# Optimization experiments

Measured on AMD Instinct MI355X. Metric: run time of the kernel, lower is better.

Reference implementation:

```python
import jax, jax.numpy as jnp
import numpy as np

B, F, N, D = 4, 5, 2048, 256


def setup_inputs() -> dict:
    key = jax.random.key(0)
    k1, k2 = jax.random.split(key)
    x = jax.random.normal(k1, (B, F, N, D), dtype=jnp.float32)
    y = jax.random.normal(k2, (B, F, N, D), dtype=jnp.float32)
    return {"x": x, "y": y}


def _weight(a, b):
    # pairwise_distance with p=2 in the original is sum((a-b)**2)**(1/(2-1)),
    # i.e. SQUARED euclidean distance (no sqrt). Use gram expansion to avoid
    # materializing the [B,F,N,N,D] difference tensor.
    a2 = jnp.sum(a * a, axis=-1)                      # [B,F,N]
    b2 = jnp.sum(b * b, axis=-1)                      # [B,F,M]
    ab = jnp.einsum('bfnd,bfmd->bfnm', a, b)          # [B,F,N,M]
    d = a2[..., :, None] + b2[..., None, :] - 2.0 * ab  # squared dists
    # min over neighbors (dim=1 of the per-frame matrix), mean over query
    # nodes, then mean over frames -> one scalar per batch element.
    return jnp.mean(jnp.min(d, axis=-1), axis=(-1, -2))  # [B]


def _normalize(f):
    # min/max over the node dim (dim=2), per (batch, frame, feature)
    mn = jnp.min(f, axis=2, keepdims=True)
    mx = jnp.max(f, axis=2, keepdims=True)
    return (f - mn) / (mx - mn)


def reference(x, y):
    wx = 1.0 / (1.0 + _weight(x, y))  # [B]
    wy = 1.0 / (1.0 + _weight(y, x))  # [B]
    nx = _normalize(x)
    ny = _normalize(y)
    return wx[:, None, None, None] * nx + wy[:, None, None, None] * ny
```

## Files before the change

### kernel.cpp

```cpp
#include <hip/hip_runtime.h>

typedef unsigned int u32;
typedef unsigned short u16;
typedef __attribute__((ext_vector_type(8))) short short8;
typedef __attribute__((ext_vector_type(4))) float floatx4;

#define NB 4
#define NF 5
#define NN 2048
#define NDM 256
#define NBF (NB*NF)
#define NBFN (NBF*NN)
#define NBFD (NBF*NDM)

#define AS1 __attribute__((address_space(1)))
#define AS3 __attribute__((address_space(3)))

__device__ u16    g_xb[(size_t)NBF*NN*NDM];
__device__ u16    g_yb[(size_t)NBF*NN*NDM];
__device__ float  g_a2[NBFN];
__device__ float  g_b2[NBFN];
__device__ float  g_rpart[(size_t)4*NBFN];
__device__ float  g_cpart[(size_t)64*NBFN];
__device__ float  g_pmn[2][(size_t)32*NBFD];
__device__ float  g_pmx[2][(size_t)32*NBFD];
__device__ float  g_bfsum[2*NBF];
__device__ float4 g_coef[NBFD];

__device__ __forceinline__ u16 cvt_bf16(float f){
  u32 b = __float_as_uint(f);
  return (u16)((b + 0x7FFFu + ((b >> 16) & 1u)) >> 16);
}
__device__ __forceinline__ float bf2f(short v){
  return __uint_as_float(((u32)(u16)v) << 16);
}
__device__ __forceinline__ void load16(const void* g, void* l){
  __builtin_amdgcn_global_load_lds((AS1 const void*)g, (AS3 void*)l, 16, 0, 0);
}

__global__ void __launch_bounds__(256) k_prep(const float* __restrict__ x,
                                              const float* __restrict__ y){
  __shared__ float sS[64][65];
  __shared__ float sp[4][64];
  __shared__ float4 smn[4][64], smx[4][64];
  int bi = blockIdx.x;
  if (bi == 0 && threadIdx.x < 2*NBF) g_bfsum[threadIdx.x] = 0.f;
  int tensor = bi >= (NBF*32); int rem = bi - tensor*(NBF*32);
  int bf = rem >> 5; int chunk = rem & 31;
  size_t rbase = (size_t)bf*NN + (size_t)chunk*64;
  const float* src = (tensor ? y : x) + rbase*NDM;
  u16*  dst  = (tensor ? g_yb : g_xb) + rbase*NDM;
  float* sums = (tensor ? g_b2 : g_a2) + bf*NN + chunk*64;
  int w = threadIdx.x >> 6, l = threadIdx.x & 63;

  float4 vmn = make_float4(INFINITY,INFINITY,INFINITY,INFINITY);
  float4 vmx = make_float4(-INFINITY,-INFINITY,-INFINITY,-INFINITY);
  for (int i = 0; i < 16; ++i){
    int row = w + 4*i;
    float4 v = ((const float4*)(src + (size_t)row*NDM))[l];
    sS[row][l] = v.x*v.x + v.y*v.y + v.z*v.z + v.w*v.w;
    ((ushort4*)(dst + (size_t)row*NDM))[l] =
        make_ushort4(cvt_bf16(v.x), cvt_bf16(v.y), cvt_bf16(v.z), cvt_bf16(v.w));
    vmn.x = fminf(vmn.x, v.x); vmn.y = fminf(vmn.y, v.y);
    vmn.z = fminf(vmn.z, v.z); vmn.w = fminf(vmn.w, v.w);
    vmx.x = fmaxf(vmx.x, v.x); vmx.y = fmaxf(vmx.y, v.y);
    vmx.z = fmaxf(vmx.z, v.z); vmx.w = fmaxf(vmx.w, v.w);
  }
  smn[w][l] = vmn; smx[w][l] = vmx;
  __syncthreads();
  {
    int row = threadIdx.x & 63, q = threadIdx.x >> 6;
    float p = 0.f;
    #pragma unroll
    for (int i = 0; i < 16; ++i) p += sS[row][q*16 + i];
    sp[q][row] = p;
  }
  __syncthreads();
  if (threadIdx.x < 64)
    sums[threadIdx.x] = sp[0][threadIdx.x] + sp[1][threadIdx.x]
                      + sp[2][threadIdx.x] + sp[3][threadIdx.x];
  if (w == 0){
    float4 a = smn[0][l], b_ = smn[1][l], c = smn[2][l], d = smn[3][l];
    float4 e = smx[0][l], f = smx[1][l], g = smx[2][l], h = smx[3][l];
    float4 mn4 = make_float4(fminf(fminf(a.x,b_.x), fminf(c.x,d.x)),
                             fminf(fminf(a.y,b_.y), fminf(c.y,d.y)),
                             fminf(fminf(a.z,b_.z), fminf(c.z,d.z)),
                             fminf(fminf(a.w,b_.w), fminf(c.w,d.w)));
    float4 mx4 = make_float4(fmaxf(fmaxf(e.x,f.x), fmaxf(g.x,h.x)),
                             fmaxf(fmaxf(e.y,f.y), fmaxf(g.y,h.y)),
                             fmaxf(fmaxf(e.z,f.z), fmaxf(g.z,h.z)),
                             fmaxf(fmaxf(e.w,f.w), fmaxf(g.w,h.w)));
    ((float4*)&g_pmn[tensor][(size_t)chunk*NBFD + bf*NDM])[l] = mn4;
    ((float4*)&g_pmx[tensor][(size_t)chunk*NBFD + bf*NDM])[l] = mx4;
  }
}

__global__ void __launch_bounds__(256, 2) k_gemm(){
  __shared__ u16 Bs[2][128*64];
  __shared__ float b2s[512];
  const int bf = blockIdx.z;
  const int i0 = blockIdx.y * 128;
  const int jq = blockIdx.x;
  const int t = threadIdx.x;
  const int w = t >> 6, l = t & 63;
  const int quad = l >> 4, c16 = l & 15;
  const int wrow = w * 32;
  const u16* xb = g_xb + (size_t)bf * NN * NDM;
  const u16* yb = g_yb + (size_t)bf * NN * NDM;

  const float* b2 = g_b2 + bf*NN;
  ((float2*)b2s)[t] = ((const float2*)(b2 + jq*512))[t];

  short8 af[2][8];
  #pragma unroll
  for (int mb = 0; mb < 2; ++mb){
    const u16* rp = xb + (size_t)(i0 + wrow + mb*16 + c16) * NDM + quad*8;
    #pragma unroll
    for (int ks = 0; ks < 8; ++ks)
      af[mb][ks] = *(const short8*)(rp + ks*32);
  }
  const float* a2 = g_a2 + bf*NN + i0 + wrow;
  float a2r[2][4];
  #pragma unroll
  for (int mb = 0; mb < 2; ++mb)
    #pragma unroll
    for (int r = 0; r < 4; ++r)
      a2r[mb][r] = a2[mb*16 + quad*4 + r];

  float rm[2][4];
  #pragma unroll
  for (int mb = 0; mb < 2; ++mb)
    #pragma unroll
    for (int r = 0; r < 4; ++r) rm[mb][r] = INFINITY;

  auto stage = [&](int it, int bb){
    const int j0 = jq*512 + (it >> 2)*128;
    const int ko = (it & 3)*64;
    #pragma unroll
    for (int q = 0; q < 4; ++q){
      const int rb = q*32 + w*8;
      const int row = rb + (l >> 3);
      const int c = (l & 7) ^ ((l >> 3) & 7);
      load16(yb + (size_t)(j0 + row)*NDM + ko + c*8,
             &Bs[bb][rb*64]);
    }
  };

  int buf = 0;
  stage(0, 0);
  for (int jj = 0; jj < 4; ++jj){
    const int j0 = jq*512 + jj*128;
    floatx4 acc[2][8] = {};
    #pragma unroll
    for (int s = 0; s < 4; ++s){
      __syncthreads();
      const int nit = jj*4 + s + 1;
      if (nit < 16) stage(nit, buf ^ 1);
      #pragma unroll
      for (int ksl = 0; ksl < 2; ++ksl){
        const int lc = ((ksl*4 + quad) ^ (c16 & 7)) * 8;
        short8 bq[8];
        #pragma unroll
        for (int nb = 0; nb < 8; ++nb)
          bq[nb] = *(const short8*)&Bs[buf][(nb*16 + c16)*64 + lc];
        #pragma unroll
        for (int mb = 0; mb < 2; ++mb)
          #pragma unroll
          for (int nb = 0; nb < 8; ++nb)
            acc[mb][nb] = __builtin_amdgcn_mfma_f32_16x16x32_bf16(af[mb][s*2+ksl], bq[nb], acc[mb][nb], 0, 0, 0);
      }
      buf ^= 1;
    }
    float bcol[8], colm[8];
    #pragma unroll
    for (int nb = 0; nb < 8; ++nb){
      bcol[nb] = b2s[jj*128 + nb*16 + c16];
      colm[nb] = INFINITY;
    }
    #pragma unroll
    for (int mb = 0; mb < 2; ++mb)
      #pragma unroll
      for (int r = 0; r < 4; ++r)
        #pragma unroll
        for (int nb = 0; nb < 8; ++nb){
          float dd = a2r[mb][r] + bcol[nb] - 2.0f * acc[mb][nb][r];
          rm[mb][r] = fminf(rm[mb][r], dd);
          colm[nb] = fminf(colm[nb], dd);
        }
    #pragma unroll
    for (int nb = 0; nb < 8; ++nb){
      float cm = colm[nb];
      cm = fminf(cm, __shfl_xor(cm, 16, 64));
      cm = fminf(cm, __shfl_xor(cm, 32, 64));
      if (quad == 0)
        g_cpart[(size_t)(blockIdx.y*4 + w)*NBFN + bf*NN + j0 + nb*16 + c16] = cm;
    }
  }
  #pragma unroll
  for (int mb = 0; mb < 2; ++mb)
    #pragma unroll
    for (int r = 0; r < 4; ++r){
      float v = rm[mb][r];
      v = fminf(v, __shfl_xor(v, 1, 64));
      v = fminf(v, __shfl_xor(v, 2, 64));
      v = fminf(v, __shfl_xor(v, 4, 64));
      v = fminf(v, __shfl_xor(v, 8, 64));
      if (c16 == 0)
        g_rpart[(size_t)jq*NBFN + bf*NN + i0 + wrow + mb*16 + quad*4 + r] = v;
    }
}

__global__ void __launch_bounds__(256) k_weight(){
  int bf = blockIdx.x >> 3;
  int chunk = blockIdx.x & 7;
  int i = chunk*256 + threadIdx.x;
  size_t base = (size_t)bf*NN + i;
  float m = INFINITY, c = INFINITY;
  #pragma unroll
  for (int p = 0; p < 4; ++p)  m = fminf(m, g_rpart[(size_t)p*NBFN + base]);
  #pragma unroll
  for (int p = 0; p < 64; ++p) c = fminf(c, g_cpart[(size_t)p*NBFN + base]);
  float srow = m, scol = c;
  #pragma unroll
  for (int mm = 1; mm < 64; mm <<= 1){
    srow += __shfl_xor(srow, mm, 64);
    scol += __shfl_xor(scol, mm, 64);
  }
  __shared__ float pr[4], pcn[4];
  int w = threadIdx.x >> 6, l = threadIdx.x & 63;
  if (l == 0){ pr[w] = srow; pcn[w] = scol; }
  __syncthreads();
  if (threadIdx.x == 0){
    atomicAdd(&g_bfsum[bf],       pr[0]+pr[1]+pr[2]+pr[3]);
    atomicAdd(&g_bfsum[NBF + bf], pcn[0]+pcn[1]+pcn[2]+pcn[3]);
  }
}

__global__ void k_coef(){
  int idx = blockIdx.x * 256 + threadIdx.x;
  int bf = idx >> 8;
  int b = bf / NF;
  float swx = 0.f, swy = 0.f;
  #pragma unroll
  for (int f = 0; f < NF; ++f){
    swx += g_bfsum[b*NF + f];
    swy += g_bfsum[NBF + b*NF + f];
  }
  float wx = 1.0f / (1.0f + swx * (1.0f/(NF*NN)));
  float wy = 1.0f / (1.0f + swy * (1.0f/(NF*NN)));
  float mnx = INFINITY, mxx = -INFINITY, mny = INFINITY, mxy = -INFINITY;
  #pragma unroll
  for (int c = 0; c < 32; ++c){
    mnx = fminf(mnx, g_pmn[0][(size_t)c*NBFD + idx]);
    mxx = fmaxf(mxx, g_pmx[0][(size_t)c*NBFD + idx]);
    mny = fminf(mny, g_pmn[1][(size_t)c*NBFD + idx]);
    mxy = fmaxf(mxy, g_pmx[1][(size_t)c*NBFD + idx]);
  }
  float sx = wx / (mxx - mnx), sy = wy / (mxy - mny);
  g_coef[idx] = make_float4(sx, -sx * mnx, sy, -sy * mny);
}

__global__ void __launch_bounds__(256) k_out(floatx4* __restrict__ out){
  size_t e0 = ((size_t)blockIdx.x * 256 + threadIdx.x) * 8;
  int bf = (int)(e0 >> 19);
  int d0 = (int)(e0 & 255);
  short8 xv = *(const short8*)&g_xb[e0];
  short8 yv = *(const short8*)&g_yb[e0];
  const float4* cf = &g_coef[bf*256 + d0];
  floatx4 o0, o1;
  #pragma unroll
  for (int j = 0; j < 4; ++j){
    float4 c = cf[j];
    o0[j] = c.x * bf2f(xv[j]) + c.y + c.z * bf2f(yv[j]) + c.w;
  }
  #pragma unroll
  for (int j = 0; j < 4; ++j){
    float4 c = cf[4 + j];
    o1[j] = c.x * bf2f(xv[4 + j]) + c.y + c.z * bf2f(yv[4 + j]) + c.w;
  }
  __builtin_nontemporal_store(o0, &out[e0 >> 2]);
  __builtin_nontemporal_store(o1, &out[(e0 >> 2) + 1]);
}

extern "C" void kernel_launch(void* const* d_in, const int* in_sizes, int n_in,
                              void* d_out, int out_size, void* d_ws, size_t ws_size,
                              hipStream_t stream) {
  const float* x = (const float*)d_in[0];
  const float* y = (const float*)d_in[1];
  (void)d_ws; (void)ws_size; (void)in_sizes; (void)n_in; (void)out_size;

  k_prep  <<<dim3(1280),      dim3(256), 0, stream>>>(x, y);
  k_gemm  <<<dim3(4, 16, 20), dim3(256), 0, stream>>>();
  k_weight<<<dim3(160),       dim3(256), 0, stream>>>();
  k_coef  <<<dim3(20),        dim3(256), 0, stream>>>();
  k_out   <<<dim3(5120),      dim3(256), 0, stream>>>((floatx4*)d_out);
}
```

Measured before the change: 220.4 us.

## Triple-buffer GEMM B tiles with explicit vmcnt waits and XCD-aware block remap

The GEMM kernel goes from double- to triple-buffered LDS staging, prefetching two stages ahead. The full __syncthreads is replaced by hand-placed s_waitcnt vmcnt counts plus a raw s_barrier, so more async loads stay in flight during the MFMA work. The grid is flattened to 1-D and remapped so consecutive blocks on the same XCD (orig & 7) handle neighbouring work items, which should improve L2 reuse of the shared x/y tiles. This costs extra LDS, which may lower occupancy, and the hand-counted waitcnts are fragile if the compiler changes how many loads it emits.

Result: no change. 224.0 us (+1.6%).

```diff
diff --git a/kernel.cpp b/kernel.cpp
--- a/kernel.cpp
+++ b/kernel.cpp
@@ -96,11 +96,14 @@
 }
 
 __global__ void __launch_bounds__(256, 2) k_gemm(){
-  __shared__ u16 Bs[2][128*64];
+  __shared__ u16 Bs[3][128*64];
   __shared__ float b2s[512];
-  const int bf = blockIdx.z;
-  const int i0 = blockIdx.y * 128;
-  const int jq = blockIdx.x;
+  const int orig = blockIdx.x;
+  const int work = (orig & 7)*160 + (orig >> 3);
+  const int bf  = work >> 6;
+  const int jq  = (work >> 4) & 3;
+  const int i0t = work & 15;
+  const int i0  = i0t * 128;
   const int t = threadIdx.x;
   const int w = t >> 6, l = t & 63;
   const int quad = l >> 4, c16 = l & 15;
@@ -146,30 +149,42 @@
     }
   };
 
-  int buf = 0;
-  stage(0, 0);
+  stage(0, 0); stage(1, 1);
   for (int jj = 0; jj < 4; ++jj){
     const int j0 = jq*512 + jj*128;
     floatx4 acc[2][8] = {};
     #pragma unroll
     for (int s = 0; s < 4; ++s){
-      __syncthreads();
-      const int nit = jj*4 + s + 1;
-      if (nit < 16) stage(nit, buf ^ 1);
+      const int it = jj*4 + s;
+      if (s == 0){
+        if (jj == 0) asm volatile("s_waitcnt vmcnt(4) lgkmcnt(0)" ::: "memory");
+        else         asm volatile("s_waitcnt vmcnt(12)" ::: "memory");
+      } else if (s == 1){
+        if (jj == 0) asm volatile("s_waitcnt vmcnt(4)" ::: "memory");
+        else         asm volatile("s_waitcnt vmcnt(12)" ::: "memory");
+      } else if (s == 3){
+        if (jj == 3) asm volatile("s_waitcnt vmcnt(0)" ::: "memory");
+        else         asm volatile("s_waitcnt vmcnt(4)" ::: "memory");
+      } else {
+        asm volatile("s_waitcnt vmcnt(4)" ::: "memory");
+      }
+      __builtin_amdgcn_s_barrier();
+      const int nit = it + 2;
+      if (nit < 16) stage(nit, nit % 3);
+      const int bufc = it % 3;
       #pragma unroll
       for (int ksl = 0; ksl < 2; ++ksl){
         const int lc = ((ksl*4 + quad) ^ (c16 & 7)) * 8;
         short8 bq[8];
         #pragma unroll
         for (int nb = 0; nb < 8; ++nb)
-          bq[nb] = *(const short8*)&Bs[buf][(nb*16 + c16)*64 + lc];
+          bq[nb] = *(const short8*)&Bs[bufc][(nb*16 + c16)*64 + lc];
         #pragma unroll
         for (int mb = 0; mb < 2; ++mb)
           #pragma unroll
           for (int nb = 0; nb < 8; ++nb)
             acc[mb][nb] = __builtin_amdgcn_mfma_f32_16x16x32_bf16(af[mb][s*2+ksl], bq[nb], acc[mb][nb], 0, 0, 0);
       }
-      buf ^= 1;
     }
     float bcol[8], colm[8];
     #pragma unroll
@@ -193,7 +208,7 @@
       cm = fminf(cm, __shfl_xor(cm, 16, 64));
       cm = fminf(cm, __shfl_xor(cm, 32, 64));
       if (quad == 0)
-        g_cpart[(size_t)(blockIdx.y*4 + w)*NBFN + bf*NN + j0 + nb*16 + c16] = cm;
+        g_cpart[(size_t)(i0t*4 + w)*NBFN + bf*NN + j0 + nb*16 + c16] = cm;
     }
   }
   #pragma unroll
@@ -289,9 +304,9 @@
   const float* y = (const float*)d_in[1];
   (void)d_ws; (void)ws_size; (void)in_sizes; (void)n_in; (void)out_size;
 
-  k_prep  <<<dim3(1280),      dim3(256), 0, stream>>>(x, y);
-  k_gemm  <<<dim3(4, 16, 20), dim3(256), 0, stream>>>();
-  k_weight<<<dim3(160),       dim3(256), 0, stream>>>();
-  k_coef  <<<dim3(20),        dim3(256), 0, stream>>>();
-  k_out   <<<dim3(5120),      dim3(256), 0, stream>>>((floatx4*)d_out);
-}
+  k_prep  <<<dim3(1280), dim3(256), 0, stream>>>(x, y);
+  k_gemm  <<<dim3(1280), dim3(256), 0, stream>>>();
+  k_weight<<<dim3(160),  dim3(256), 0, stream>>>();
+  k_coef  <<<dim3(20),   dim3(256), 0, stream>>>();
+  k_out   <<<dim3(5120), dim3(256), 0, stream>>>((floatx4*)d_out);
+}
```
